# Performance work log

Hardware: AMD Instinct MI355X
Metric: run time of the kernel (lower is better)

## Reference

```python
import jax, jax.numpy as jnp
import numpy as np

N_NODES = 50000
N_EDGES = 800000
NFEAT, NHID, IN_HEAD, NCLASS, OUT_HEAD = 256, 16, 8, 47, 1
NEG_SLOPE = 0.2


def setup_inputs() -> dict:
    key = jax.random.key(0)
    ks = jax.random.split(key, 10)
    x = jax.random.normal(ks[0], (N_NODES, NFEAT), dtype=jnp.float32)
    edge_index = jax.random.randint(ks[1], (2, N_EDGES), 0, N_NODES, dtype=jnp.int64)
    W1 = jax.random.normal(ks[2], (NFEAT, IN_HEAD * NHID), dtype=jnp.float32) * 0.06
    a1_src = jax.random.normal(ks[3], (IN_HEAD, NHID), dtype=jnp.float32) * 0.25
    a1_dst = jax.random.normal(ks[4], (IN_HEAD, NHID), dtype=jnp.float32) * 0.25
    b1 = jax.random.normal(ks[5], (IN_HEAD * NHID,), dtype=jnp.float32) * 0.02
    W2 = jax.random.normal(ks[6], (IN_HEAD * NHID, NCLASS), dtype=jnp.float32) * 0.09
    a2_src = jax.random.normal(ks[7], (OUT_HEAD, NCLASS), dtype=jnp.float32) * 0.15
    a2_dst = jax.random.normal(ks[8], (OUT_HEAD, NCLASS), dtype=jnp.float32) * 0.15
    b2 = jax.random.normal(ks[9], (NCLASS,), dtype=jnp.float32) * 0.02
    return {"x": x, "edge_index": edge_index, "W1": W1, "a1_src": a1_src,
            "a1_dst": a1_dst, "b1": b1, "W2": W2, "a2_src": a2_src,
            "a2_dst": a2_dst, "b2": b2}


def _gat_layer(x, W, a_src, a_dst, b, src, dst, n_nodes, concat):
    # x: [N, F_in]; W: [F_in, H*C]; a_*: [H, C]
    H, C = a_src.shape
    h = (x @ W).reshape(n_nodes, H, C)                        # [N, H, C]
    # per-node partial attention logits, then gather per edge
    s_src = jnp.einsum('nhc,hc->nh', h, a_src)                # [N, H]
    s_dst = jnp.einsum('nhc,hc->nh', h, a_dst)                # [N, H]
    e = jax.nn.leaky_relu(s_src[src] + s_dst[dst], NEG_SLOPE) # [E, H]
    # segment softmax over destination node
    m = jax.ops.segment_max(e, dst, num_segments=n_nodes)     # [N, H]
    ex = jnp.exp(e - m[dst])
    denom = jax.ops.segment_sum(ex, dst, num_segments=n_nodes)
    alpha = ex / (denom[dst] + 1e-16)                         # [E, H]
    # weighted message aggregation (scatter-add)
    msg = alpha[:, :, None] * h[src]                          # [E, H, C]
    out = jax.ops.segment_sum(msg, dst, num_segments=n_nodes) # [N, H, C]
    out = out.reshape(n_nodes, H * C) if concat else out.mean(axis=1)
    return out + b


def reference(x, edge_index, W1, a1_src, a1_dst, b1, W2, a2_src, a2_dst, b2):
    n = x.shape[0]
    # PyG GATConv default: add self-loops
    loops = jnp.arange(n, dtype=edge_index.dtype)
    src = jnp.concatenate([edge_index[0], loops])
    dst = jnp.concatenate([edge_index[1], loops])
    # eval mode: dropout is identity
    h = _gat_layer(x, W1, a1_src, a1_dst, b1, src, dst, n, concat=True)
    h = jax.nn.elu(h)
    out = _gat_layer(h, W2, a2_src, a2_dst, b2, src, dst, n, concat=False)
    return jax.nn.log_softmax(out, axis=1)
```

## Files before the change

### kernel.cpp

```cpp
#include <hip/hip_runtime.h>
#include <hip/hip_fp16.h>

#define N_NODES 50000
#define N_EDGES 800000
#define E2 (N_EDGES + N_NODES)

#define BSHIFT 6
#define BMASK 63
#define NBUCK 782
#define GRPS 8
#define SUBCAP 256
#define BUCKCAP (GRPS * SUBCAP)
#define CURPAD 32

typedef _Float16 h8v __attribute__((ext_vector_type(8)));
typedef float f4v __attribute__((ext_vector_type(4)));


__global__ __launch_bounds__(256) void k_gscatter(const int* __restrict__ ei,
        int* __restrict__ bcur, unsigned int* __restrict__ brec) {
    int e = blockIdx.x * 256 + threadIdx.x;
    if (e >= E2) return;
    int src, dst;
    if (e < N_EDGES) { src = ei[e]; dst = ei[N_EDGES + e]; }
    else             { src = dst = e - N_EDGES; }
    int b = dst >> BSHIFT;
    int g = blockIdx.x & (GRPS - 1);
    int pos = atomicAdd(&bcur[(b * GRPS + g) * CURPAD], 1);
    if (pos < SUBCAP)
        brec[b * BUCKCAP + g * SUBCAP + pos] =
            ((unsigned int)(dst & BMASK) << 16) | (unsigned int)src;
}

__global__ __launch_bounds__(1024) void k_segscan(const int* __restrict__ bcur,
        int* __restrict__ boff, const float* __restrict__ W2, float* __restrict__ W2p) {
    int t = threadIdx.x;
    for (int i = t; i < 128 * 48; i += 1024) {
        int k = i / 48, c = i - k * 48;
        W2p[i] = (c < 47) ? W2[k * 47 + c] : 0.f;
    }
    int v = 0;
    if (t < NBUCK) {
        #pragma unroll
        for (int g = 0; g < GRPS; ++g) {
            int c = bcur[(t * GRPS + g) * CURPAD];
            v += (c < SUBCAP) ? c : SUBCAP;
        }
    }
    __shared__ int ws[16];
    int lane = t & 63, w = t >> 6;
    int x = v;
    #pragma unroll
    for (int o = 1; o < 64; o <<= 1) { int y = __shfl_up(x, o); if (lane >= o) x += y; }
    if (lane == 63) ws[w] = x;
    __syncthreads();
    if (t == 0) {
        #pragma unroll
        for (int j = 1; j < 16; ++j) ws[j] += ws[j - 1];
    }
    __syncthreads();
    int add = (w == 0) ? 0 : ws[w - 1];
    int excl = add + x - v;
    if (t < NBUCK) boff[t] = excl;
    if (t == NBUCK - 1) boff[NBUCK] = excl + v;
}

__global__ __launch_bounds__(256) void k_finalize(const unsigned int* __restrict__ brec,
        const int* __restrict__ bcur, const int* __restrict__ boff,
        unsigned short* __restrict__ csr_src, int* __restrict__ offs) {
    int B = blockIdx.x;
    int tid = threadIdx.x;
    __shared__ int hist[64], cur[64], cnt_s[GRPS];
    __shared__ unsigned short stage[BUCKCAP];
    if (tid < 64) hist[tid] = 0;
    if (tid < GRPS) {
        int c = bcur[(B * GRPS + tid) * CURPAD];
        cnt_s[tid] = (c < SUBCAP) ? c : SUBCAP;
    }
    __syncthreads();
    const unsigned int* bp = brec + (size_t)B * BUCKCAP;
    #pragma unroll
    for (int g = 0; g < GRPS; ++g) {
        int c = cnt_s[g];
        for (int i = tid; i < c; i += 256) atomicAdd(&hist[bp[g * SUBCAP + i] >> 16], 1);
    }
    __syncthreads();
    int base = boff[B];
    if (tid < 64) {
        int v = hist[tid];
        int x = v;
        #pragma unroll
        for (int o = 1; o < 64; o <<= 1) { int y = __shfl_up(x, o); if (tid >= o) x += y; }
        int excl = x - v;
        cur[tid] = excl;
        int n = B * 64 + tid;
        if (n < N_NODES) offs[n] = base + excl;
    }
    if (B == NBUCK - 1 && tid == 0) offs[N_NODES] = boff[NBUCK];
    __syncthreads();
    #pragma unroll
    for (int g = 0; g < GRPS; ++g) {
        int c = cnt_s[g];
        for (int i = tid; i < c; i += 256) {
            unsigned int r = bp[g * SUBCAP + i];
            int p = atomicAdd(&cur[r >> 16], 1);
            stage[p] = (unsigned short)(r & 0xFFFFu);
        }
    }
    __syncthreads();
    int total = boff[B + 1] - base;
    for (int i = tid; i < total; i += 256) csr_src[base + i] = stage[i];
}


__global__ void k_prepw1(const float* __restrict__ W1, _Float16* __restrict__ W1T) {
    int i = blockIdx.x * 256 + threadIdx.x;
    if (i >= 128 * 256) return;
    int c = i >> 8, k = i & 255;
    W1T[i] = (_Float16)W1[k * 128 + c];
}


__global__ __launch_bounds__(128) void k_gemm1(const float* __restrict__ x,
        const _Float16* __restrict__ W1T, _Float16* __restrict__ h1h) {
    int lane = threadIdx.x & 63;
    int wv = threadIdx.x >> 6;
    int rowbase = blockIdx.x * 64 + wv * 32;
    int r0 = lane & 15;
    int kg = lane >> 4;
    f4v acc[2][8];
    #pragma unroll
    for (int i = 0; i < 2; ++i)
        #pragma unroll
        for (int j = 0; j < 8; ++j) acc[i][j] = (f4v)0.f;

    #pragma unroll 1
    for (int kt = 0; kt < 256; kt += 32) {
        h8v a[2];
        #pragma unroll
        for (int rf = 0; rf < 2; ++rf) {
            int row = rowbase + rf * 16 + r0;
            if (row >= N_NODES) row = N_NODES - 1;
            const float* ap = x + (size_t)row * 256 + kt + kg * 8;
            float4 lo = *(const float4*)ap;
            float4 hi = *(const float4*)(ap + 4);
            h8v t;
            t[0] = (_Float16)lo.x; t[1] = (_Float16)lo.y;
            t[2] = (_Float16)lo.z; t[3] = (_Float16)lo.w;
            t[4] = (_Float16)hi.x; t[5] = (_Float16)hi.y;
            t[6] = (_Float16)hi.z; t[7] = (_Float16)hi.w;
            a[rf] = t;
        }
        #pragma unroll
        for (int cf = 0; cf < 8; ++cf) {
            h8v b = *(const h8v*)(W1T + (size_t)(cf * 16 + r0) * 256 + kt + kg * 8);
            acc[0][cf] = __builtin_amdgcn_mfma_f32_16x16x32_f16(a[0], b, acc[0][cf], 0, 0, 0);
            acc[1][cf] = __builtin_amdgcn_mfma_f32_16x16x32_f16(a[1], b, acc[1][cf], 0, 0, 0);
        }
    }
    #pragma unroll
    for (int rf = 0; rf < 2; ++rf) {
        #pragma unroll
        for (int r = 0; r < 4; ++r) {
            int row = rowbase + rf * 16 + kg * 4 + r;
            if (row < N_NODES) {
                _Float16* orow = h1h + (size_t)row * 128 + r0;
                #pragma unroll
                for (int cf = 0; cf < 8; ++cf)
                    orow[cf * 16] = (_Float16)acc[rf][cf][r];
            }
        }
    }
}


__global__ void k_logits1(const __half* __restrict__ h1h,
                          const float* __restrict__ a1s, const float* __restrict__ a1d,
                          float* __restrict__ s1s, float* __restrict__ s1d) {
    int idx = blockIdx.x * blockDim.x + threadIdx.x;
    if (idx >= N_NODES * 8) return;
    int n = idx >> 3, h = idx & 7;
    const __half2* hp2 = (const __half2*)(h1h + (size_t)n * 128 + h * 16);
    float ss = 0.f, sd = 0.f;
    #pragma unroll
    for (int c2 = 0; c2 < 8; ++c2) {
        float2 v = __half22float2(hp2[c2]);
        ss += v.x * a1s[h * 16 + 2 * c2] + v.y * a1s[h * 16 + 2 * c2 + 1];
        sd += v.x * a1d[h * 16 + 2 * c2] + v.y * a1d[h * 16 + 2 * c2 + 1];
    }
    s1s[idx] = ss;
    s1d[idx] = sd;
}


__global__ __launch_bounds__(256) void k_agg1(const __half* __restrict__ h1h,
        const float* __restrict__ s1s, const float* __restrict__ s1d,
        const int* __restrict__ offs, const unsigned short* __restrict__ csr_src,
        const float* __restrict__ b1, float* __restrict__ h2o) {
    int wave = threadIdx.x >> 6;
    int lane = threadIdx.x & 63;
    int n = blockIdx.x * 4 + wave;
    int beg = offs[n];
    int deg = offs[n + 1] - beg;

    int h = lane & 7;
    int slot = lane >> 3;
    int hd = lane >> 3;
    float sdh = s1d[n * 8 + h];

    float dsum = 0.f;
    float accx = 0.f, accy = 0.f;
    for (int chunk = 0; chunk < deg; chunk += 8) {
        int i = chunk + slot;
        int esrc = csr_src[beg + ((i < deg) ? i : (deg - 1))];
        float aN = 0.f;
        if (i < deg) {
            float e = s1s[esrc * 8 + h] + sdh;
            e = (e > 0.f) ? e : 0.2f * e;
            aN = __expf(e);
            dsum += aN;
        }
        int   srcs[8];
        float as[8];
        #pragma unroll
        for (int s = 0; s < 8; ++s) {
            srcs[s] = __shfl(esrc, s * 8);
            as[s]   = __shfl(aN, s * 8 + hd);
        }
        __half2 v[8];
        #pragma unroll
        for (int s = 0; s < 8; ++s)
            v[s] = *(const __half2*)(h1h + (size_t)srcs[s] * 128 + 2 * lane);
        #pragma unroll
        for (int s = 0; s < 8; ++s) {
            float2 vf = __half22float2(v[s]);
            accx += as[s] * vf.x;
            accy += as[s] * vf.y;
        }
    }
    dsum += __shfl_xor(dsum, 8);
    dsum += __shfl_xor(dsum, 16);
    dsum += __shfl_xor(dsum, 32);
    float rd = 1.f / __shfl(dsum, hd);

    float v0 = accx * rd + b1[2 * lane];
    v0 = (v0 > 0.f) ? v0 : (__expf(v0) - 1.f);
    float v1 = accy * rd + b1[2 * lane + 1];
    v1 = (v1 > 0.f) ? v1 : (__expf(v1) - 1.f);
    *(float2*)(h2o + (size_t)n * 128 + 2 * lane) = make_float2(v0, v1);
}


__global__ __launch_bounds__(256) void k_gemm2(const float* __restrict__ h2,
        const float* __restrict__ W2p,
        const float* __restrict__ a2s, const float* __restrict__ a2d,
        __half* __restrict__ g2h, float* __restrict__ s2s, float* __restrict__ s2d) {
    int n = blockIdx.x * 256 + threadIdx.x;
    bool valid = (n < N_NODES);
    int nn = valid ? n : (N_NODES - 1);
    const float* hrow = h2 + (size_t)nn * 128;
    float4 acc[12];
    #pragma unroll
    for (int j = 0; j < 12; ++j) acc[j] = make_float4(0.f, 0.f, 0.f, 0.f);
    #pragma unroll 1
    for (int k = 0; k < 128; k += 4) {
        float4 hv = *(const float4*)(hrow + k);
        float hk[4] = {hv.x, hv.y, hv.z, hv.w};
        #pragma unroll
        for (int kk = 0; kk < 4; ++kk) {
            const float* wrow = W2p + (size_t)(k + kk) * 48;
            #pragma unroll
            for (int j = 0; j < 12; ++j) {
                float4 wv = *(const float4*)(wrow + j * 4);
                acc[j].x += hk[kk] * wv.x;
                acc[j].y += hk[kk] * wv.y;
                acc[j].z += hk[kk] * wv.z;
                acc[j].w += hk[kk] * wv.w;
            }
        }
    }
    float vs = 0.f, vd = 0.f;
    #pragma unroll
    for (int j = 0; j < 12; ++j) {
        int c = j * 4;
        vs += acc[j].x * a2s[c + 0]; vd += acc[j].x * a2d[c + 0];
        vs += acc[j].y * a2s[c + 1]; vd += acc[j].y * a2d[c + 1];
        vs += acc[j].z * a2s[c + 2]; vd += acc[j].z * a2d[c + 2];
        if (j < 11) { vs += acc[j].w * a2s[c + 3]; vd += acc[j].w * a2d[c + 3]; }
    }
    if (valid) {
        __half2* orow = (__half2*)(g2h + (size_t)n * 48);
        #pragma unroll
        for (int j = 0; j < 12; ++j) {
            orow[j * 2 + 0] = __floats2half2_rn(acc[j].x, acc[j].y);
            orow[j * 2 + 1] = __floats2half2_rn(acc[j].z, acc[j].w);
        }
        s2s[n] = vs;
        s2d[n] = vd;
    }
}


__global__ __launch_bounds__(256) void k_agg2(const __half* __restrict__ g2h,
        const float* __restrict__ s2s, const float* __restrict__ s2d,
        const int* __restrict__ offs, const unsigned short* __restrict__ csr_src,
        const float* __restrict__ b2, float* __restrict__ outp) {
    int wave = threadIdx.x >> 6, lane = threadIdx.x & 63;
    int n = blockIdx.x * 4 + wave;
    int beg = offs[n];
    int deg = offs[n + 1] - beg;
    float sdn = s2d[n];
    int c = (lane < 47) ? lane : 47;

    float dsum = 0.f;
    float acc = 0.f;
    for (int chunk = 0; chunk < deg; chunk += 64) {
        int i = chunk + lane;
        int esrc = csr_src[beg + ((i < deg) ? i : (deg - 1))];
        float aN = 0.f;
        if (i < deg) {
            float e = s2s[esrc] + sdn;
            e = (e > 0.f) ? e : 0.2f * e;
            aN = __expf(e);
            dsum += aN;
        }
        int lim = deg - chunk; if (lim > 64) lim = 64;
        for (int g = 0; g < lim; g += 8) {
            int   srcs[8];
            float as[8];
            #pragma unroll
            for (int s = 0; s < 8; ++s) {
                srcs[s] = __shfl(esrc, g + s);
                as[s]   = __shfl(aN, g + s);
            }
            __half v[8];
            #pragma unroll
            for (int s = 0; s < 8; ++s) v[s] = g2h[(size_t)srcs[s] * 48 + c];
            #pragma unroll
            for (int s = 0; s < 8; ++s) acc += as[s] * __half2float(v[s]);
        }
    }
    #pragma unroll
    for (int o = 32; o; o >>= 1) dsum += __shfl_xor(dsum, o);
    acc *= 1.f / dsum;

    float l = (lane < 47) ? acc + b2[lane] : -1e30f;
    float rm = l;
    #pragma unroll
    for (int o = 32; o; o >>= 1) rm = fmaxf(rm, __shfl_xor(rm, o));
    float p = (lane < 47) ? __expf(l - rm) : 0.f;
    float ps = p;
    #pragma unroll
    for (int o = 32; o; o >>= 1) ps += __shfl_xor(ps, o);
    float lse = rm + __logf(ps);
    if (lane < 47) outp[(size_t)n * 47 + lane] = l - lse;
}


extern "C" void kernel_launch(void* const* d_in, const int* in_sizes, int n_in,
                              void* d_out, int out_size, void* d_ws, size_t ws_size,
                              hipStream_t stream) {
    const float* x   = (const float*)d_in[0];
    const int*   ei  = (const int*)d_in[1];
    const float* W1  = (const float*)d_in[2];
    const float* a1s = (const float*)d_in[3];
    const float* a1d = (const float*)d_in[4];
    const float* b1  = (const float*)d_in[5];
    const float* W2  = (const float*)d_in[6];
    const float* a2s = (const float*)d_in[7];
    const float* a2d = (const float*)d_in[8];
    const float* b2  = (const float*)d_in[9];
    float* outp = (float*)d_out;

    char* ws = (char*)d_ws;
    size_t off = 0;
    auto alloc = [&](size_t bytes) -> void* {
        void* p = ws + off;
        off += (bytes + 255) & ~(size_t)255;
        return p;
    };
    int* bcur    = (int*)alloc((size_t)NBUCK * GRPS * CURPAD * 4);
    int* boff    = (int*)alloc((size_t)(NBUCK + 1) * 4);
    unsigned int* brec = (unsigned int*)alloc((size_t)NBUCK * BUCKCAP * 4);
    unsigned short* csr_src = (unsigned short*)alloc((size_t)E2 * 2);
    int* offs    = (int*)alloc((size_t)(N_NODES + 1) * 4);
    __half* h1h  = (__half*)alloc((size_t)N_NODES * 128 * 2);
    float* s1s   = (float*)alloc((size_t)N_NODES * 8 * 4);
    float* s1d   = (float*)alloc((size_t)N_NODES * 8 * 4);
    float* h2    = (float*)alloc((size_t)N_NODES * 128 * 4);
    __half* g2h  = (__half*)alloc((size_t)N_NODES * 48 * 2);
    float* s2s   = (float*)alloc((size_t)N_NODES * 4);
    float* s2d   = (float*)alloc((size_t)N_NODES * 4);
    float* W2p   = (float*)alloc((size_t)128 * 48 * 4);
    _Float16* W1T = (_Float16*)alloc((size_t)128 * 256 * 2);

    (void)in_sizes; (void)n_in; (void)out_size; (void)ws_size;

    hipMemsetAsync(bcur, 0, (size_t)NBUCK * GRPS * CURPAD * 4, stream);
    k_prepw1<<<128, 256, 0, stream>>>(W1, W1T);
    k_gscatter<<<(E2 + 255) / 256, 256, 0, stream>>>(ei, bcur, brec);
    k_segscan<<<1, 1024, 0, stream>>>(bcur, boff, W2, W2p);
    k_finalize<<<NBUCK, 256, 0, stream>>>(brec, bcur, boff, csr_src, offs);

    k_gemm1<<<(N_NODES + 63) / 64, 128, 0, stream>>>(x, W1T, (_Float16*)h1h);
    k_logits1<<<(N_NODES * 8 + 255) / 256, 256, 0, stream>>>(h1h, a1s, a1d, s1s, s1d);
    k_agg1<<<N_NODES / 4, 256, 0, stream>>>(h1h, s1s, s1d, offs, csr_src, b1, h2);

    k_gemm2<<<(N_NODES + 255) / 256, 256, 0, stream>>>(h2, W2p, a2s, a2d, g2h, s2s, s2d);
    k_agg2<<<N_NODES / 4, 256, 0, stream>>>(g2h, s2s, s2d, offs, csr_src, b2, outp);
}
```

Before: 219.2 us.

## Pick scatter sub-bucket by XCC id and add overflow path for full sub-buckets

The edge bucketing kernel now picks the sub-bucket counter by the hardware XCC id instead of the block index, so atomics from one XCC land on counters that XCC owns, which is meant to cut cross-die atomic traffic. Because sub-bucket loads can now be uneven, edges past a sub-bucket's capacity go to a global overflow buffer. The scan and finalize kernels fold those overflow edges back in, which adds an extra memset, an overflow scan in every finalize block, and a direct-write fallback for buckets larger than the staging area. Before this change, edges past capacity were silently dropped.

```diff
diff --git a/kernel.cpp b/kernel.cpp
--- a/kernel.cpp
+++ b/kernel.cpp
@@ -16,29 +16,46 @@
 typedef _Float16 h8v __attribute__((ext_vector_type(8)));
 typedef float f4v __attribute__((ext_vector_type(4)));
 
+__device__ __forceinline__ int xcc_id() {
+    return (int)__builtin_amdgcn_s_getreg(20 | (0 << 6) | ((4 - 1) << 11)) & (GRPS - 1);
+}
+
 
 __global__ __launch_bounds__(256) void k_gscatter(const int* __restrict__ ei,
-        int* __restrict__ bcur, unsigned int* __restrict__ brec) {
+        int* __restrict__ bcur, unsigned int* __restrict__ brec,
+        int* __restrict__ ocnt, unsigned int* __restrict__ obuf) {
     int e = blockIdx.x * 256 + threadIdx.x;
     if (e >= E2) return;
     int src, dst;
     if (e < N_EDGES) { src = ei[e]; dst = ei[N_EDGES + e]; }
     else             { src = dst = e - N_EDGES; }
     int b = dst >> BSHIFT;
-    int g = blockIdx.x & (GRPS - 1);
+    int g = xcc_id();
     int pos = atomicAdd(&bcur[(b * GRPS + g) * CURPAD], 1);
-    if (pos < SUBCAP)
+    if (pos < SUBCAP) {
         brec[b * BUCKCAP + g * SUBCAP + pos] =
             ((unsigned int)(dst & BMASK) << 16) | (unsigned int)src;
+    } else {
+        int op = atomicAdd(ocnt, 1);
+        obuf[op] = ((unsigned int)dst << 16) | (unsigned int)src;
+    }
 }
 
 __global__ __launch_bounds__(1024) void k_segscan(const int* __restrict__ bcur,
-        int* __restrict__ boff, const float* __restrict__ W2, float* __restrict__ W2p) {
+        int* __restrict__ boff, const float* __restrict__ W2, float* __restrict__ W2p,
+        const int* __restrict__ ocnt, const unsigned int* __restrict__ obuf) {
     int t = threadIdx.x;
     for (int i = t; i < 128 * 48; i += 1024) {
         int k = i / 48, c = i - k * 48;
         W2p[i] = (c < 47) ? W2[k * 47 + c] : 0.f;
     }
+    __shared__ int ovh[NBUCK];
+    for (int i = t; i < NBUCK; i += 1024) ovh[i] = 0;
+    __syncthreads();
+    int oc = *ocnt;
+    for (int i = t; i < oc; i += 1024)
+        atomicAdd(&ovh[(obuf[i] >> 16) >> BSHIFT], 1);
+    __syncthreads();
     int v = 0;
     if (t < NBUCK) {
         #pragma unroll
@@ -46,6 +63,7 @@
             int c = bcur[(t * GRPS + g) * CURPAD];
             v += (c < SUBCAP) ? c : SUBCAP;
         }
+        v += ovh[t];
     }
     __shared__ int ws[16];
     int lane = t & 63, w = t >> 6;
@@ -67,7 +85,8 @@
 
 __global__ __launch_bounds__(256) void k_finalize(const unsigned int* __restrict__ brec,
         const int* __restrict__ bcur, const int* __restrict__ boff,
-        unsigned short* __restrict__ csr_src, int* __restrict__ offs) {
+        unsigned short* __restrict__ csr_src, int* __restrict__ offs,
+        const int* __restrict__ ocnt, const unsigned int* __restrict__ obuf) {
     int B = blockIdx.x;
     int tid = threadIdx.x;
     __shared__ int hist[64], cur[64], cnt_s[GRPS];
@@ -84,8 +103,16 @@
         int c = cnt_s[g];
         for (int i = tid; i < c; i += 256) atomicAdd(&hist[bp[g * SUBCAP + i] >> 16], 1);
     }
+    int oc = *ocnt;
+    if (oc > 0) {
+        for (int i = tid; i < oc; i += 256) {
+            unsigned int r = obuf[i];
+            if ((int)((r >> 16) >> BSHIFT) == B) atomicAdd(&hist[(r >> 16) & BMASK], 1);
+        }
+    }
     __syncthreads();
     int base = boff[B];
+    int total = boff[B + 1] - base;
     if (tid < 64) {
         int v = hist[tid];
         int x = v;
@@ -98,18 +125,47 @@
     }
     if (B == NBUCK - 1 && tid == 0) offs[N_NODES] = boff[NBUCK];
     __syncthreads();
-    #pragma unroll
-    for (int g = 0; g < GRPS; ++g) {
-        int c = cnt_s[g];
-        for (int i = tid; i < c; i += 256) {
-            unsigned int r = bp[g * SUBCAP + i];
-            int p = atomicAdd(&cur[r >> 16], 1);
-            stage[p] = (unsigned short)(r & 0xFFFFu);
-        }
-    }
-    __syncthreads();
-    int total = boff[B + 1] - base;
-    for (int i = tid; i < total; i += 256) csr_src[base + i] = stage[i];
+    if (total <= BUCKCAP) {
+        #pragma unroll
+        for (int g = 0; g < GRPS; ++g) {
+            int c = cnt_s[g];
+            for (int i = tid; i < c; i += 256) {
+                unsigned int r = bp[g * SUBCAP + i];
+                int p = atomicAdd(&cur[r >> 16], 1);
+                stage[p] = (unsigned short)(r & 0xFFFFu);
+            }
+        }
+        if (oc > 0) {
+            for (int i = tid; i < oc; i += 256) {
+                unsigned int r = obuf[i];
+                if ((int)((r >> 16) >> BSHIFT) == B) {
+                    int p = atomicAdd(&cur[(r >> 16) & BMASK], 1);
+                    stage[p] = (unsigned short)(r & 0xFFFFu);
+                }
+            }
+        }
+        __syncthreads();
+        for (int i = tid; i < total; i += 256) csr_src[base + i] = stage[i];
+    } else {
+        #pragma unroll
+        for (int g = 0; g < GRPS; ++g) {
+            int c = cnt_s[g];
+            for (int i = tid; i < c; i += 256) {
+                unsigned int r = bp[g * SUBCAP + i];
+                int p = atomicAdd(&cur[r >> 16], 1);
+                csr_src[base + p] = (unsigned short)(r & 0xFFFFu);
+            }
+        }
+        if (oc > 0) {
+            for (int i = tid; i < oc; i += 256) {
+                unsigned int r = obuf[i];
+                if ((int)((r >> 16) >> BSHIFT) == B) {
+                    int p = atomicAdd(&cur[(r >> 16) & BMASK], 1);
+                    csr_src[base + p] = (unsigned short)(r & 0xFFFFu);
+                }
+            }
+        }
+    }
 }
 
 
@@ -384,6 +440,8 @@
     unsigned int* brec = (unsigned int*)alloc((size_t)NBUCK * BUCKCAP * 4);
     unsigned short* csr_src = (unsigned short*)alloc((size_t)E2 * 2);
     int* offs    = (int*)alloc((size_t)(N_NODES + 1) * 4);
+    int* ocnt    = (int*)alloc(256);
+    unsigned int* obuf = (unsigned int*)alloc((size_t)E2 * 4);
     __half* h1h  = (__half*)alloc((size_t)N_NODES * 128 * 2);
     float* s1s   = (float*)alloc((size_t)N_NODES * 8 * 4);
     float* s1d   = (float*)alloc((size_t)N_NODES * 8 * 4);
@@ -397,10 +455,11 @@
     (void)in_sizes; (void)n_in; (void)out_size; (void)ws_size;
 
     hipMemsetAsync(bcur, 0, (size_t)NBUCK * GRPS * CURPAD * 4, stream);
+    hipMemsetAsync(ocnt, 0, 4, stream);
     k_prepw1<<<128, 256, 0, stream>>>(W1, W1T);
-    k_gscatter<<<(E2 + 255) / 256, 256, 0, stream>>>(ei, bcur, brec);
-    k_segscan<<<1, 1024, 0, stream>>>(bcur, boff, W2, W2p);
-    k_finalize<<<NBUCK, 256, 0, stream>>>(brec, bcur, boff, csr_src, offs);
+    k_gscatter<<<(E2 + 255) / 256, 256, 0, stream>>>(ei, bcur, brec, ocnt, obuf);
+    k_segscan<<<1, 1024, 0, stream>>>(bcur, boff, W2, W2p, ocnt, obuf);
+    k_finalize<<<NBUCK, 256, 0, stream>>>(brec, bcur, boff, csr_src, offs, ocnt, obuf);
 
     k_gemm1<<<(N_NODES + 63) / 64, 128, 0, stream>>>(x, W1T, (_Float16*)h1h);
     k_logits1<<<(N_NODES * 8 + 255) / 256, 256, 0, stream>>>(h1h, a1s, a1d, s1s, s1d);
```

Result: no change. 223.0 us (+1.8%).

## Replace atomic bucket scatter with two-pass histogram and scan counting sort

Applied to the files above, without the earlier changes.

Swaps the single-pass global-atomic bucket scatter, which used capped sub-buckets and a memset, for a counting sort. Each of 208 blocks builds a shared-memory histogram over 4096 edges, a column scan turns these into per-block bucket offsets, and a placement pass writes compact bucket records using only shared-memory atomics. This removes global atomic contention and the fixed-capacity bucket layout, and it also removes the silent truncation when a sub-bucket overflowed. The cost is two extra kernel launches and reading the edge list twice. The finalize kernel gains a fallback that writes directly to global memory for buckets too large for shared staging.

```diff
diff --git a/kernel.cpp b/kernel.cpp
--- a/kernel.cpp
+++ b/kernel.cpp
@@ -8,45 +8,57 @@
 #define BSHIFT 6
 #define BMASK 63
 #define NBUCK 782
-#define GRPS 8
-#define SUBCAP 256
-#define BUCKCAP (GRPS * SUBCAP)
-#define CURPAD 32
+#define EPB 4096
+#define NBLKC 208
 
 typedef _Float16 h8v __attribute__((ext_vector_type(8)));
 typedef float f4v __attribute__((ext_vector_type(4)));
 
 
-__global__ __launch_bounds__(256) void k_gscatter(const int* __restrict__ ei,
-        int* __restrict__ bcur, unsigned int* __restrict__ brec) {
-    int e = blockIdx.x * 256 + threadIdx.x;
-    if (e >= E2) return;
-    int src, dst;
-    if (e < N_EDGES) { src = ei[e]; dst = ei[N_EDGES + e]; }
-    else             { src = dst = e - N_EDGES; }
-    int b = dst >> BSHIFT;
-    int g = blockIdx.x & (GRPS - 1);
-    int pos = atomicAdd(&bcur[(b * GRPS + g) * CURPAD], 1);
-    if (pos < SUBCAP)
-        brec[b * BUCKCAP + g * SUBCAP + pos] =
-            ((unsigned int)(dst & BMASK) << 16) | (unsigned int)src;
-}
-
-__global__ __launch_bounds__(1024) void k_segscan(const int* __restrict__ bcur,
+__global__ __launch_bounds__(256) void k_hist(const int* __restrict__ ei,
+                                              int* __restrict__ gh) {
+    __shared__ int h[NBUCK];
+    int tid = threadIdx.x;
+    for (int b = tid; b < NBUCK; b += 256) h[b] = 0;
+    __syncthreads();
+    int base = blockIdx.x * EPB;
+    for (int i = tid; i < EPB; i += 256) {
+        int e = base + i;
+        if (e < E2) {
+            int dst = (e < N_EDGES) ? ei[N_EDGES + e] : (e - N_EDGES);
+            atomicAdd(&h[dst >> BSHIFT], 1);
+        }
+    }
+    __syncthreads();
+    for (int b = tid; b < NBUCK; b += 256) gh[blockIdx.x * NBUCK + b] = h[b];
+}
+
+__global__ __launch_bounds__(256) void k_colscan(int* __restrict__ gh,
+                                                 int* __restrict__ tot) {
+    int wave = threadIdx.x >> 6, lane = threadIdx.x & 63;
+    int b = blockIdx.x * 4 + wave;
+    if (b >= NBUCK) return;
+    int carry = 0;
+    for (int c = 0; c < NBLKC; c += 64) {
+        int k = c + lane;
+        int v = (k < NBLKC) ? gh[k * NBUCK + b] : 0;
+        int x = v;
+        #pragma unroll
+        for (int o = 1; o < 64; o <<= 1) { int y = __shfl_up(x, o); if (lane >= o) x += y; }
+        if (k < NBLKC) gh[k * NBUCK + b] = carry + x - v;
+        carry += __shfl(x, 63);
+    }
+    if (lane == 0) tot[b] = carry;
+}
+
+__global__ __launch_bounds__(1024) void k_btot(const int* __restrict__ tot,
         int* __restrict__ boff, const float* __restrict__ W2, float* __restrict__ W2p) {
     int t = threadIdx.x;
     for (int i = t; i < 128 * 48; i += 1024) {
         int k = i / 48, c = i - k * 48;
         W2p[i] = (c < 47) ? W2[k * 47 + c] : 0.f;
     }
-    int v = 0;
-    if (t < NBUCK) {
-        #pragma unroll
-        for (int g = 0; g < GRPS; ++g) {
-            int c = bcur[(t * GRPS + g) * CURPAD];
-            v += (c < SUBCAP) ? c : SUBCAP;
-        }
-    }
+    int v = (t < NBUCK) ? tot[t] : 0;
     __shared__ int ws[16];
     int lane = t & 63, w = t >> 6;
     int x = v;
@@ -65,27 +77,45 @@
     if (t == NBUCK - 1) boff[NBUCK] = excl + v;
 }
 
+__global__ __launch_bounds__(256) void k_place(const int* __restrict__ ei,
+        const int* __restrict__ gh, const int* __restrict__ boff,
+        unsigned int* __restrict__ brec) {
+    __shared__ int sbase[NBUCK];
+    __shared__ int cnt[NBUCK];
+    int tid = threadIdx.x;
+    for (int b = tid; b < NBUCK; b += 256) {
+        sbase[b] = boff[b] + gh[blockIdx.x * NBUCK + b];
+        cnt[b] = 0;
+    }
+    __syncthreads();
+    int base = blockIdx.x * EPB;
+    for (int i = tid; i < EPB; i += 256) {
+        int e = base + i;
+        if (e < E2) {
+            int src, dst;
+            if (e < N_EDGES) { src = ei[e]; dst = ei[N_EDGES + e]; }
+            else             { src = dst = e - N_EDGES; }
+            int b = dst >> BSHIFT;
+            int r = atomicAdd(&cnt[b], 1);
+            brec[sbase[b] + r] = ((unsigned int)(dst & BMASK) << 16) | (unsigned int)src;
+        }
+    }
+}
+
 __global__ __launch_bounds__(256) void k_finalize(const unsigned int* __restrict__ brec,
-        const int* __restrict__ bcur, const int* __restrict__ boff,
-        unsigned short* __restrict__ csr_src, int* __restrict__ offs) {
+        const int* __restrict__ boff, unsigned short* __restrict__ csr_src,
+        int* __restrict__ offs) {
     int B = blockIdx.x;
     int tid = threadIdx.x;
-    __shared__ int hist[64], cur[64], cnt_s[GRPS];
-    __shared__ unsigned short stage[BUCKCAP];
+    int base = boff[B];
+    int total = boff[B + 1] - base;
+    __shared__ int hist[64], cur[64];
+    __shared__ unsigned short stage[2048];
     if (tid < 64) hist[tid] = 0;
-    if (tid < GRPS) {
-        int c = bcur[(B * GRPS + tid) * CURPAD];
-        cnt_s[tid] = (c < SUBCAP) ? c : SUBCAP;
-    }
-    __syncthreads();
-    const unsigned int* bp = brec + (size_t)B * BUCKCAP;
-    #pragma unroll
-    for (int g = 0; g < GRPS; ++g) {
-        int c = cnt_s[g];
-        for (int i = tid; i < c; i += 256) atomicAdd(&hist[bp[g * SUBCAP + i] >> 16], 1);
-    }
-    __syncthreads();
-    int base = boff[B];
+    __syncthreads();
+    const unsigned int* bp = brec + base;
+    for (int i = tid; i < total; i += 256) atomicAdd(&hist[bp[i] >> 16], 1);
+    __syncthreads();
     if (tid < 64) {
         int v = hist[tid];
         int x = v;
@@ -98,18 +128,21 @@
     }
     if (B == NBUCK - 1 && tid == 0) offs[N_NODES] = boff[NBUCK];
     __syncthreads();
-    #pragma unroll
-    for (int g = 0; g < GRPS; ++g) {
-        int c = cnt_s[g];
-        for (int i = tid; i < c; i += 256) {
-            unsigned int r = bp[g * SUBCAP + i];
+    if (total <= 2048) {
+        for (int i = tid; i < total; i += 256) {
+            unsigned int r = bp[i];
             int p = atomicAdd(&cur[r >> 16], 1);
             stage[p] = (unsigned short)(r & 0xFFFFu);
         }
-    }
-    __syncthreads();
-    int total = boff[B + 1] - base;
-    for (int i = tid; i < total; i += 256) csr_src[base + i] = stage[i];
+        __syncthreads();
+        for (int i = tid; i < total; i += 256) csr_src[base + i] = stage[i];
+    } else {
+        for (int i = tid; i < total; i += 256) {
+            unsigned int r = bp[i];
+            int p = atomicAdd(&cur[r >> 16], 1);
+            csr_src[base + p] = (unsigned short)(r & 0xFFFFu);
+        }
+    }
 }
 
 
@@ -379,9 +412,10 @@
         off += (bytes + 255) & ~(size_t)255;
         return p;
     };
-    int* bcur    = (int*)alloc((size_t)NBUCK * GRPS * CURPAD * 4);
+    int* gh      = (int*)alloc((size_t)NBLKC * NBUCK * 4);
+    int* tot     = (int*)alloc((size_t)NBUCK * 4);
     int* boff    = (int*)alloc((size_t)(NBUCK + 1) * 4);
-    unsigned int* brec = (unsigned int*)alloc((size_t)NBUCK * BUCKCAP * 4);
+    unsigned int* brec = (unsigned int*)alloc((size_t)E2 * 4);
     unsigned short* csr_src = (unsigned short*)alloc((size_t)E2 * 2);
     int* offs    = (int*)alloc((size_t)(N_NODES + 1) * 4);
     __half* h1h  = (__half*)alloc((size_t)N_NODES * 128 * 2);
@@ -396,11 +430,12 @@
 
     (void)in_sizes; (void)n_in; (void)out_size; (void)ws_size;
 
-    hipMemsetAsync(bcur, 0, (size_t)NBUCK * GRPS * CURPAD * 4, stream);
     k_prepw1<<<128, 256, 0, stream>>>(W1, W1T);
-    k_gscatter<<<(E2 + 255) / 256, 256, 0, stream>>>(ei, bcur, brec);
-    k_segscan<<<1, 1024, 0, stream>>>(bcur, boff, W2, W2p);
-    k_finalize<<<NBUCK, 256, 0, stream>>>(brec, bcur, boff, csr_src, offs);
+    k_hist<<<NBLKC, 256, 0, stream>>>(ei, gh);
+    k_colscan<<<(NBUCK + 3) / 4, 256, 0, stream>>>(gh, tot);
+    k_btot<<<1, 1024, 0, stream>>>(tot, boff, W2, W2p);
+    k_place<<<NBLKC, 256, 0, stream>>>(ei, gh, boff, brec);
+    k_finalize<<<NBUCK, 256, 0, stream>>>(brec, boff, csr_src, offs);
 
     k_gemm1<<<(N_NODES + 63) / 64, 128, 0, stream>>>(x, W1T, (_Float16*)h1h);
     k_logits1<<<(N_NODES * 8 + 255) / 256, 256, 0, stream>>>(h1h, a1s, a1d, s1s, s1d);
```

New measurement: 181.5 us. -17.2%, faster.
